# Optimization experiments

Measured on AMD Instinct MI355X. Metric: run time of the kernel, lower is better.

## Reference

```python
import jax, jax.numpy as jnp
import numpy as np

B, T, IN, H = 32, 128, 256, 512      # batch, time, input, hidden
N, R, W = 128, 4, 64                  # mem cells, read heads, cell width
RW = R * W
FOUT = 256
IF = R * W + 3 * W + 5 * R + 3        # DNC interface vector size
EPS = 1e-6


def setup_inputs() -> dict:
    k = jax.random.split(jax.random.key(0), 9)
    g = lambda kk, sh, fan: jax.random.normal(kk, sh, jnp.float32) / np.sqrt(fan).astype(np.float32)
    return {
        "x": jax.random.normal(k[0], (B, T, IN), jnp.float32),
        "W_ih": g(k[1], (4 * H, IN + RW), IN + RW),
        "W_hh": g(k[2], (4 * H, H), H),
        "b_ih": jnp.zeros((4 * H,), jnp.float32),
        "b_hh": jnp.zeros((4 * H,), jnp.float32),
        "W_if": g(k[3], (IF, H), H),
        "b_if": jnp.zeros((IF,), jnp.float32),
        "W_emb": g(k[4], (FOUT, H + RW), H + RW),
        "b_emb": jnp.zeros((FOUT,), jnp.float32),
    }


def _content(keys, strengths, mem):
    # keys (b,k,w), strengths (b,k), mem (b,n,w) -> softmax cosine addressing (b,k,n)
    kn = keys / (jnp.linalg.norm(keys, axis=-1, keepdims=True) + EPS)
    mn = mem / (jnp.linalg.norm(mem, axis=-1, keepdims=True) + EPS)
    sim = jnp.einsum('bkw,bnw->bkn', kn, mn)
    return jax.nn.softmax(sim * strengths[..., None], axis=-1)


def _dnc_forward(x, W_ih, W_hh, b_ih, b_hh, W_if, b_if, W_emb, b_emb):
    b = x.shape[0]
    eye = jnp.eye(N, dtype=x.dtype)

    def step(carry, x_t):
        h, c, mem, link, prec, read_w, write_w, usage, last_read = carry
        # LSTM controller step on [x_t, last_read] (pytorch gate order i,f,g,o)
        inp = jnp.concatenate([x_t, last_read], axis=-1)
        gates = inp @ W_ih.T + h @ W_hh.T + b_ih + b_hh
        i, f, g_, o = jnp.split(gates, 4, axis=-1)
        c = jax.nn.sigmoid(f) * c + jax.nn.sigmoid(i) * jnp.tanh(g_)
        h = jax.nn.sigmoid(o) * jnp.tanh(c)

        # interface vector
        xi = h @ W_if.T + b_if
        off = 0
        read_keys = jnp.tanh(xi[:, :R * W].reshape(b, R, W)); off = R * W
        read_str = jax.nn.softplus(xi[:, off:off + R]); off += R
        write_key = jnp.tanh(xi[:, off:off + W]); off += W
        write_str = jax.nn.softplus(xi[:, off:off + 1]); off += 1
        erase = jax.nn.sigmoid(xi[:, off:off + W]); off += W
        write_vec = jnp.tanh(xi[:, off:off + W]); off += W
        free_g = jax.nn.sigmoid(xi[:, off:off + R]); off += R
        alloc_g = jax.nn.sigmoid(xi[:, off:off + 1]); off += 1
        write_g = jax.nn.sigmoid(xi[:, off:off + 1]); off += 1
        read_modes = jax.nn.softmax(xi[:, off:off + 3 * R].reshape(b, R, 3), axis=-1)

        # usage update + allocation weighting (sort / cumprod / scatter-back)
        psi = jnp.prod(1.0 - free_g[:, :, None] * read_w, axis=1)          # (b,n) retention
        usage = (usage + write_w - usage * write_w) * psi
        order = jnp.argsort(usage, axis=1)                                  # free-list order
        sorted_u = jnp.take_along_axis(usage, order, axis=1)
        cp = jnp.cumprod(jnp.concatenate([jnp.ones((b, 1), usage.dtype), sorted_u[:, :-1]], axis=1), axis=1)
        a_sorted = (1.0 - sorted_u) * cp
        alloc = jnp.zeros_like(usage).at[jnp.arange(b)[:, None], order].set(a_sorted)

        # write weighting + memory update
        cw = _content(write_key[:, None, :], write_str, mem)[:, 0]          # (b,n)
        write_w = write_g * (alloc_g * alloc + (1.0 - alloc_g) * cw)
        mem = mem * (1.0 - write_w[:, :, None] * erase[:, None, :]) + write_w[:, :, None] * write_vec[:, None, :]

        # temporal link matrix + precedence
        link = (1.0 - write_w[:, :, None] - write_w[:, None, :]) * link + write_w[:, :, None] * prec[:, None, :]
        link = link * (1.0 - eye)
        prec = (1.0 - jnp.sum(write_w, axis=1, keepdims=True)) * prec + write_w

        # read weighting: backward / content / forward modes
        fwd = jnp.einsum('bnm,brm->brn', link, read_w)
        bwd = jnp.einsum('bmn,brm->brn', link, read_w)
        cr = _content(read_keys, read_str, mem)
        read_w = read_modes[..., 0:1] * bwd + read_modes[..., 1:2] * cr + read_modes[..., 2:3] * fwd
        read_vecs = jnp.einsum('brn,bnw->brw', read_w, mem)
        last_read = read_vecs.reshape(b, RW)

        out = jnp.concatenate([h, last_read], axis=-1) @ W_emb.T + b_emb
        return (h, c, mem, link, prec, read_w, write_w, usage, last_read), out

    z = jnp.zeros
    carry0 = (z((b, H)), z((b, H)), z((b, N, W)), z((b, N, N)), z((b, N)),
              z((b, R, N)), z((b, N)), z((b, N)), z((b, RW)))
    _, outs = jax.lax.scan(step, carry0, jnp.swapaxes(x, 0, 1))
    return jnp.swapaxes(outs, 0, 1)  # (b, T, FOUT)


def reference(x, W_ih, W_hh, b_ih, b_hh, W_if, b_if, W_emb, b_emb):
    return _dnc_forward(x, W_ih, W_hh, b_ih, b_hh, W_if, b_if, W_emb, b_emb)
```

## Files before the change

kernel.cpp:

```cpp
#include <hip/hip_runtime.h>
#include <math.h>

#define B_    32
#define T_    128
#define IN_   256
#define H_    512
#define N_    128
#define R_    4
#define W_    64
#define RW_   256
#define FOUT_ 256
#define IF_   471
#define XIP   480
#define EPSF  1e-6f
#define KPAD  260
#define NBLK  208

typedef float v4f __attribute__((ext_vector_type(4)));

#define OFF_H0    0
#define OFF_H1    16384
#define OFF_LR    32768
#define OFF_XI    40960
#define OFF_FLAGA (OFF_XI + 32*XIP)
#define OFF_FLAGX (OFF_FLAGA + 144*32)
#define OFF_FLAGC (OFF_FLAGX + 32*32)
#define WS_TOTAL  (OFF_FLAGC + 32*32)

__device__ __forceinline__ float sig_(float x)   { return 1.0f / (1.0f + expf(-x)); }
__device__ __forceinline__ float splus_(float x) { return fmaxf(x, 0.0f) + log1pf(expf(-fabsf(x))); }

__device__ __forceinline__ void cstore(float* p, float v) {
    __hip_atomic_store(p, v, __ATOMIC_RELAXED, __HIP_MEMORY_SCOPE_AGENT);
}
__device__ __forceinline__ unsigned uload(const unsigned* p) {
    return __hip_atomic_load(p, __ATOMIC_RELAXED, __HIP_MEMORY_SCOPE_AGENT);
}
__device__ __forceinline__ void ustore(unsigned* p, unsigned v) {
    __hip_atomic_store(p, v, __ATOMIC_RELAXED, __HIP_MEMORY_SCOPE_AGENT);
}
__device__ __forceinline__ void cload4x4(const float* p0, const float* p1,
                                         const float* p2, const float* p3,
                                         v4f& a, v4f& b, v4f& c, v4f& d) {
    asm volatile(
        "global_load_dwordx4 %0, %4, off sc0 sc1\n\t"
        "global_load_dwordx4 %1, %5, off sc0 sc1\n\t"
        "global_load_dwordx4 %2, %6, off sc0 sc1\n\t"
        "global_load_dwordx4 %3, %7, off sc0 sc1\n\t"
        "s_waitcnt vmcnt(0)"
        : "=&v"(a), "=&v"(b), "=&v"(c), "=&v"(d)
        : "v"(p0), "v"(p1), "v"(p2), "v"(p3)
        : "memory");
}
__device__ __forceinline__ v4f cload4(const float* p) {
    v4f v;
    asm volatile("global_load_dwordx4 %0, %1, off sc0 sc1\n\ts_waitcnt vmcnt(0)"
                 : "=&v"(v) : "v"(p) : "memory");
    return v;
}
__device__ __forceinline__ void cstore4(float* p, v4f v) {
    asm volatile("global_store_dwordx4 %0, %1, off sc0 sc1" :: "v"(p), "v"(v) : "memory");
}

__device__ __forceinline__ unsigned long long shflx64(unsigned long long v, int m) {
    unsigned int lo = (unsigned int)v, hi = (unsigned int)(v >> 32);
    lo = (unsigned int)__shfl_xor((int)lo, m);
    hi = (unsigned int)__shfl_xor((int)hi, m);
    return ((unsigned long long)hi << 32) | lo;
}

__global__ void k_init(float* p, int n) {
    for (int i = blockIdx.x * blockDim.x + threadIdx.x; i < n; i += gridDim.x * blockDim.x)
        p[i] = 0.0f;
}

__device__ __forceinline__ void post_flag(unsigned* slot, unsigned val) {
    asm volatile("s_waitcnt vmcnt(0)" ::: "memory");
    __syncthreads();
    if (threadIdx.x == 0) ustore(slot, val);
}

struct SA {
    float act[32 * KPAD];
    float sg[4][4][32];
    float cc[4][32];
    float hst[4][32];
};
struct SM {
    float link[N_][N_ + 1];
    float mem[N_ * (W_ + 1)];
    float sxi[XIP];
    float rw[R_*N_], fwd[R_*N_], bwd[R_*N_], cr[R_*N_];
    float cw[N_], usage[N_], alloc[N_], wwv[N_], prc[N_], minv[N_];
    float rkeys[R_*W_], wkey[W_], ev[W_], wv[W_];
    float rstr[R_], fg[R_], kinv[R_], m1[R_], modes[R_*3], sc[8];
    unsigned long long key[N_];
};

__device__ __forceinline__ void stage_coh(const float* __restrict__ src, int rowstride,
                                          int colofs, float* lds, int tid) {
    int f0 = 0*256 + tid, f1 = 1*256 + tid, f2 = 2*256 + tid, f3 = 3*256 + tid;
    int f4 = 4*256 + tid, f5 = 5*256 + tid, f6 = 6*256 + tid, f7 = 7*256 + tid;
    const float* p0 = src + (size_t)(f0 >> 6) * rowstride + colofs + ((f0 & 63) << 2);
    const float* p1 = src + (size_t)(f1 >> 6) * rowstride + colofs + ((f1 & 63) << 2);
    const float* p2 = src + (size_t)(f2 >> 6) * rowstride + colofs + ((f2 & 63) << 2);
    const float* p3 = src + (size_t)(f3 >> 6) * rowstride + colofs + ((f3 & 63) << 2);
    const float* p4 = src + (size_t)(f4 >> 6) * rowstride + colofs + ((f4 & 63) << 2);
    const float* p5 = src + (size_t)(f5 >> 6) * rowstride + colofs + ((f5 & 63) << 2);
    const float* p6 = src + (size_t)(f6 >> 6) * rowstride + colofs + ((f6 & 63) << 2);
    const float* p7 = src + (size_t)(f7 >> 6) * rowstride + colofs + ((f7 & 63) << 2);
    v4f r0, r1, r2, r3, r4, r5, r6, r7;
    cload4x4(p0, p1, p2, p3, r0, r1, r2, r3);
    cload4x4(p4, p5, p6, p7, r4, r5, r6, r7);
    *reinterpret_cast<v4f*>(&lds[(f0 >> 6) * KPAD + ((f0 & 63) << 2)]) = r0;
    *reinterpret_cast<v4f*>(&lds[(f1 >> 6) * KPAD + ((f1 & 63) << 2)]) = r1;
    *reinterpret_cast<v4f*>(&lds[(f2 >> 6) * KPAD + ((f2 & 63) << 2)]) = r2;
    *reinterpret_cast<v4f*>(&lds[(f3 >> 6) * KPAD + ((f3 & 63) << 2)]) = r3;
    *reinterpret_cast<v4f*>(&lds[(f4 >> 6) * KPAD + ((f4 & 63) << 2)]) = r4;
    *reinterpret_cast<v4f*>(&lds[(f5 >> 6) * KPAD + ((f5 & 63) << 2)]) = r5;
    *reinterpret_cast<v4f*>(&lds[(f6 >> 6) * KPAD + ((f6 & 63) << 2)]) = r6;
    *reinterpret_cast<v4f*>(&lds[(f7 >> 6) * KPAD + ((f7 & 63) << 2)]) = r7;
}
__device__ __forceinline__ void stage_x(const float* __restrict__ x, int t, float* lds, int tid) {
    #pragma unroll
    for (int i = 0; i < 8; ++i) {
        int f = i * 256 + tid;
        int b = f >> 6, k4 = (f & 63) << 2;
        v4f v = *reinterpret_cast<const v4f*>(x + ((size_t)b * T_ + t) * IN_ + k4);
        *reinterpret_cast<v4f*>(&lds[b * KPAD + k4]) = v;
    }
}

__device__ __forceinline__ void tile_mac4(const float* lds,
        const float* __restrict__ w0p, const float* __restrict__ w1p,
        const float* __restrict__ w2p, const float* __restrict__ w3p,
        int lane, float* v)
{
    v4f w0 = *reinterpret_cast<const v4f*>(w0p + lane * 4);
    v4f w1 = *reinterpret_cast<const v4f*>(w1p + lane * 4);
    v4f w2 = *reinterpret_cast<const v4f*>(w2p + lane * 4);
    v4f w3 = *reinterpret_cast<const v4f*>(w3p + lane * 4);
    #pragma unroll
    for (int b = 0; b < 32; ++b) {
        v4f a = *reinterpret_cast<const v4f*>(lds + b * KPAD + lane * 4);
        v[0*32+b] = fmaf(w0.w, a.w, fmaf(w0.z, a.z, fmaf(w0.y, a.y, fmaf(w0.x, a.x, v[0*32+b]))));
        v[1*32+b] = fmaf(w1.w, a.w, fmaf(w1.z, a.z, fmaf(w1.y, a.y, fmaf(w1.x, a.x, v[1*32+b]))));
        v[2*32+b] = fmaf(w2.w, a.w, fmaf(w2.z, a.z, fmaf(w2.y, a.y, fmaf(w2.x, a.x, v[2*32+b]))));
        v[3*32+b] = fmaf(w3.w, a.w, fmaf(w3.z, a.z, fmaf(w3.y, a.y, fmaf(w3.x, a.x, v[3*32+b]))));
    }
}

__device__ __forceinline__ void fold128(float* v, int lane) {
    #define FOLD_STAGE(D, HALF) { _Pragma("unroll") \
        for (int i = 0; i < HALF; ++i) { \
            float a_ = v[i], c_ = v[i + HALF]; \
            float t_ = (lane & D) ? a_ : c_; \
            t_ = __shfl_xor(t_, D); \
            v[i] = (lane & D) ? (c_ + t_) : (a_ + t_); } }
    FOLD_STAGE(32, 64) FOLD_STAGE(16, 32) FOLD_STAGE(8, 16)
    FOLD_STAGE(4, 8)   FOLD_STAGE(2, 4)   FOLD_STAGE(1, 2)
    #undef FOLD_STAGE
}

__device__ void mem_body(SM& sm, int b, int tid,
        const float* __restrict__ gxi, float* __restrict__ glr)
{
    const int lane = tid & 63, wid = tid >> 6;

    if (tid < 120) {
        v4f v4 = cload4(&gxi[(size_t)b * XIP + tid * 4]);
        *reinterpret_cast<v4f*>(&sm.sxi[tid * 4]) = v4;
    }
    __syncthreads();

    for (int i = tid; i < IF_; i += 256) {
        float vv = sm.sxi[i];
        if      (i < 256) sm.rkeys[i]     = tanhf(vv);
        else if (i < 260) sm.rstr[i-256]  = splus_(vv);
        else if (i < 324) sm.wkey[i-260]  = tanhf(vv);
        else if (i < 325) sm.sc[0]        = splus_(vv);
        else if (i < 389) sm.ev[i-325]    = sig_(vv);
        else if (i < 453) sm.wv[i-389]    = tanhf(vv);
        else if (i < 457) sm.fg[i-453]    = sig_(vv);
        else if (i < 458) sm.sc[1]        = sig_(vv);
        else if (i < 459) sm.sc[2]        = sig_(vv);
        else              sm.modes[i-459] = vv;
    }
    __syncthreads();

    unsigned long long key = ~0ull;
    if (tid < N_) {
        float p = 1.0f;
        #pragma unroll
        for (int r = 0; r < R_; ++r) p *= 1.0f - sm.fg[r] * sm.rw[r*N_ + tid];
        float uo = sm.usage[tid], w0 = sm.wwv[tid];
        float u = (uo + w0 - uo*w0) * p;
        sm.usage[tid] = u;
        unsigned int fb = __float_as_uint(u);
        fb = (fb & 0x80000000u) ? ~fb : (fb | 0x80000000u);
        key = ((unsigned long long)fb << 32) | (unsigned int)tid;
        float s = 0.0f;
        for (int w = 0; w < W_; ++w) { float m = sm.mem[tid*(W_+1)+w]; s += m*m; }
        sm.minv[tid] = 1.0f / (sqrtf(s) + EPSF);
    }
    if (tid >= 128 && tid < 128 + R_) {
        int r = tid - 128;
        float s = 0.0f;
        for (int w = 0; w < W_; ++w) { float kv = sm.rkeys[r*W_+w]; s += kv*kv; }
        sm.kinv[r] = 1.0f / (sqrtf(s) + EPSF);
    }
    if (tid == 132) {
        float s = 0.0f;
        for (int w = 0; w < W_; ++w) s += sm.wkey[w]*sm.wkey[w];
        sm.sc[5] = 1.0f / (sqrtf(s) + EPSF);
    }
    if (tid >= 136 && tid < 136 + R_) {
        int r = tid - 136;
        float m0 = sm.modes[r*3], m1 = sm.modes[r*3+1], m2 = sm.modes[r*3+2];
        float mx = fmaxf(m0, fmaxf(m1, m2));
        float e0 = expf(m0-mx), e1 = expf(m1-mx), e2 = expf(m2-mx);
        float inv = 1.0f / (e0 + e1 + e2);
        sm.modes[r*3] = e0*inv; sm.modes[r*3+1] = e1*inv; sm.modes[r*3+2] = e2*inv;
    }
    __syncthreads();

    if (tid < N_) {
        float d = 0.0f;
        for (int w = 0; w < W_; ++w) d += sm.wkey[w] * sm.mem[tid*(W_+1)+w];
        sm.cw[tid] = d * sm.minv[tid] * sm.sc[5] * sm.sc[0];
    }
    for (int k = 2; k <= N_; k <<= 1) {
        for (int j = k >> 1; j > 0; j >>= 1) {
            unsigned long long pk;
            if (j == 64) {
                if (tid < N_) sm.key[tid] = key;
                __syncthreads();
                pk = (tid < N_) ? sm.key[tid ^ 64] : key;
                __syncthreads();
            } else {
                pk = shflx64(key, j);
            }
            bool lower = (tid & j) == 0;
            bool asc   = (tid & k) == 0;
            if ((key > pk) == (lower == asc)) key = pk;
        }
    }

    float su = 0.0f, ex = 1.0f; int sidx = 0;
    if (tid < N_) {
        sidx = (int)(key & 0xffffffffu);
        su = sm.usage[sidx];
        float p = su;
        #pragma unroll
        for (int off = 1; off < 64; off <<= 1) {
            float pv = __shfl_up(p, off);
            if (lane >= off) p *= pv;
        }
        if (tid == 63) sm.sc[7] = p;
        float e = __shfl_up(p, 1);
        ex = (lane == 0) ? 1.0f : e;
    }
    __syncthreads();
    if (tid < N_) {
        if (tid >= 64) ex *= sm.sc[7];
        sm.alloc[sidx] = (1.0f - su) * ex;
    }
    if (wid == 2) {
        float v0 = sm.cw[lane], v1 = sm.cw[lane+64];
        float m = fmaxf(v0, v1);
        #pragma unroll
        for (int o = 32; o >= 1; o >>= 1) m = fmaxf(m, __shfl_xor(m, o));
        float e0 = expf(v0 - m), e1 = expf(v1 - m);
        float s = e0 + e1;
        #pragma unroll
        for (int o = 32; o >= 1; o >>= 1) s += __shfl_xor(s, o);
        sm.cw[lane] = e0; sm.cw[lane+64] = e1;
        if (lane == 0) sm.sc[4] = 1.0f / s;
    }
    __syncthreads();

    if (tid < N_) {
        float cwn = sm.cw[tid] * sm.sc[4];
        sm.wwv[tid] = sm.sc[2] * (sm.sc[1] * sm.alloc[tid] + (1.0f - sm.sc[1]) * cwn);
    }
    __syncthreads();

    for (int i = tid; i < N_*W_; i += 256) {
        int n = i >> 6, w = i & 63;
        float m = sm.mem[n*(W_+1)+w];
        sm.mem[n*(W_+1)+w] = m * (1.0f - sm.wwv[n]*sm.ev[w]) + sm.wwv[n]*sm.wv[w];
    }
    if (wid == 3) {
        float s = sm.wwv[lane] + sm.wwv[lane+64];
        #pragma unroll
        for (int o = 32; o >= 1; o >>= 1) s += __shfl_xor(s, o);
        if (lane == 0) sm.sc[6] = s;
    }
    __syncthreads();

    for (int i = tid; i < N_*N_; i += 256) {
        int row = i >> 7, col = i & 127;
        float wwr = sm.wwv[row];
        float nv = (1.0f - wwr - sm.wwv[col]) * sm.link[row][col] + wwr * sm.prc[col];
        if (row == col) nv = 0.0f;
        sm.link[row][col] = nv;
    }
    __syncthreads();

    for (int i = tid; i < R_*N_; i += 256) {
        int r = i >> 7, q = i & 127;
        float accf = 0.0f, accb = 0.0f;
        #pragma unroll 4
        for (int m2 = 0; m2 < 128; ++m2) {
            float rv = sm.rw[r*N_ + m2];
            accf = fmaf(sm.link[q][m2], rv, accf);
            accb = fmaf(sm.link[m2][q], rv, accb);
        }
        sm.fwd[i] = accf;
        sm.bwd[i] = accb;
    }
    __syncthreads();

    if (tid < N_) {
        sm.prc[tid] = (1.0f - sm.sc[6]) * sm.prc[tid] + sm.wwv[tid];
        float s = 0.0f;
        for (int w = 0; w < W_; ++w) { float m = sm.mem[tid*(W_+1)+w]; s += m*m; }
        sm.minv[tid] = 1.0f / (sqrtf(s) + EPSF);
    }
    __syncthreads();

    for (int i = tid; i < R_*N_; i += 256) {
        int r = i >> 7, n = i & 127;
        float d = 0.0f;
        for (int w = 0; w < W_; ++w) d += sm.rkeys[r*W_+w] * sm.mem[n*(W_+1)+w];
        sm.cr[i] = d * sm.minv[n] * sm.kinv[r] * sm.rstr[r];
    }
    __syncthreads();

    {
        int r = wid;
        float v0 = sm.cr[r*N_ + lane], v1 = sm.cr[r*N_ + lane + 64];
        float m = fmaxf(v0, v1);
        #pragma unroll
        for (int o = 32; o >= 1; o >>= 1) m = fmaxf(m, __shfl_xor(m, o));
        float e0 = expf(v0 - m), e1 = expf(v1 - m);
        float s = e0 + e1;
        #pragma unroll
        for (int o = 32; o >= 1; o >>= 1) s += __shfl_xor(s, o);
        sm.cr[r*N_ + lane] = e0; sm.cr[r*N_ + lane + 64] = e1;
        if (lane == 0) sm.m1[r] = sm.modes[r*3+1] / s;
    }
    __syncthreads();

    for (int i = tid; i < R_*N_; i += 256) {
        int r = i >> 7;
        sm.rw[i] = sm.modes[r*3] * sm.bwd[i] + sm.m1[r] * sm.cr[i] + sm.modes[r*3+2] * sm.fwd[i];
    }
    __syncthreads();

    for (int i = tid; i < R_*W_; i += 256) {
        int r = i >> 6, w = i & 63;
        float d = 0.0f;
        for (int n = 0; n < N_; ++n) d += sm.rw[r*N_ + n] * sm.mem[n*(W_+1)+w];
        cstore(&glr[(size_t)b * RW_ + i], d);
    }
}

__global__ __launch_bounds__(256, 1) void k_fused(
        const float* __restrict__ x, const float* __restrict__ Wih,
        const float* __restrict__ Whh, const float* __restrict__ bih,
        const float* __restrict__ bhh, const float* __restrict__ Wif,
        const float* __restrict__ bif, const float* __restrict__ Wemb,
        const float* __restrict__ bemb, float* __restrict__ out,
        float* __restrict__ ws)
{
    __shared__ __align__(16) char smem_raw[(sizeof(SM) > sizeof(SA)) ? sizeof(SM) : sizeof(SA)];
    SA& sa = *reinterpret_cast<SA*>(smem_raw);
    SM& sm = *reinterpret_cast<SM*>(smem_raw);

    const int bid = blockIdx.x, tid = threadIdx.x;
    const int lane = tid & 63, wid = tid >> 6;

    float* h0  = ws + OFF_H0;
    float* h1  = ws + OFF_H1;
    float* lr  = ws + OFF_LR;
    float* gxi = ws + OFF_XI;
    unsigned* flagA = (unsigned*)(ws + OFF_FLAGA);
    unsigned* flagX = (unsigned*)(ws + OFF_FLAGX);
    unsigned* flagC = (unsigned*)(ws + OFF_FLAGC);

    if (bid < 128) {
        const int j = bid * 4 + wid;
        if (tid < 128) sa.cc[tid >> 5][tid & 31] = 0.0f;
        float b0 = bih[j]        + bhh[j];
        float b1 = bih[H_ + j]   + bhh[H_ + j];
        float b2 = bih[2*H_ + j] + bhh[2*H_ + j];
        float b3 = bih[3*H_ + j] + bhh[3*H_ + j];
        __syncthreads();

        for (int t = 0; t < T_; ++t) {
            const float* hprev = (t & 1) ? h1 : h0;
            float*       hnew  = (t & 1) ? h0 : h1;
            float v[128];
            #pragma unroll
            for (int i = 0; i < 128; ++i) v[i] = 0.0f;

            stage_x(x, t, sa.act, tid);
            __syncthreads();
            tile_mac4(sa.act, Wih + (size_t)(0*H_+j)*512, Wih + (size_t)(1*H_+j)*512,
                              Wih + (size_t)(2*H_+j)*512, Wih + (size_t)(3*H_+j)*512, lane, v);
            if (tid < 128) { while (uload(&flagA[tid*32]) < (unsigned)t) __builtin_amdgcn_s_sleep(8); }
            __syncthreads();
            stage_coh(hprev, H_, 0, sa.act, tid);
            __syncthreads();
            tile_mac4(sa.act, Whh + (size_t)(0*H_+j)*512, Whh + (size_t)(1*H_+j)*512,
                              Whh + (size_t)(2*H_+j)*512, Whh + (size_t)(3*H_+j)*512, lane, v);
            __syncthreads();
            stage_coh(hprev, H_, 256, sa.act, tid);
            __syncthreads();
            tile_mac4(sa.act, Whh + (size_t)(0*H_+j)*512 + 256, Whh + (size_t)(1*H_+j)*512 + 256,
                              Whh + (size_t)(2*H_+j)*512 + 256, Whh + (size_t)(3*H_+j)*512 + 256, lane, v);
            if (tid < 32) { while (uload(&flagC[tid*32]) < (unsigned)t) __builtin_amdgcn_s_sleep(8); }
            __syncthreads();
            stage_coh(lr, RW_, 0, sa.act, tid);
            __syncthreads();
            tile_mac4(sa.act, Wih + (size_t)(0*H_+j)*512 + 256, Wih + (size_t)(1*H_+j)*512 + 256,
                              Wih + (size_t)(2*H_+j)*512 + 256, Wih + (size_t)(3*H_+j)*512 + 256, lane, v);
            fold128(v, lane);
            int r = (lane >> 4) & 3, bb0 = (lane & 15) * 2;
            sa.sg[wid][r][bb0]     = v[0];
            sa.sg[wid][r][bb0 + 1] = v[1];
            __syncthreads();
            if (lane < 32) {
                int b = lane;
                float ai = sa.sg[wid][0][b] + b0;
                float af = sa.sg[wid][1][b] + b1;
                float ag = sa.sg[wid][2][b] + b2;
                float ao = sa.sg[wid][3][b] + b3;
                float ig = sig_(ai), fg = sig_(af), gg = tanhf(ag), og = sig_(ao);
                float cn = fg * sa.cc[wid][b] + ig * gg;
                sa.cc[wid][b] = cn;
                sa.hst[wid][b] = og * tanhf(cn);
            }
            __syncthreads();
            if (tid < 32) {
                int b = tid;
                v4f hv;
                hv.x = sa.hst[0][b]; hv.y = sa.hst[1][b];
                hv.z = sa.hst[2][b]; hv.w = sa.hst[3][b];
                cstore4(&hnew[(size_t)b * H_ + bid * 4], hv);
            }
            post_flag(&flagA[bid * 32], (unsigned)(t + 1));
        }
    } else if (bid < 144) {
        const int rb = (bid - 128) * 16 + wid * 4;
        const float* w0 = Wemb + (size_t)(rb + 0) * 768;
        const float* w1 = Wemb + (size_t)(rb + 1) * 768;
        const float* w2 = Wemb + (size_t)(rb + 2) * 768;
        const float* w3 = Wemb + (size_t)(rb + 3) * 768;

        for (int t = 0; t < T_; ++t) {
            const float* hprev = (t & 1) ? h1 : h0;
            if (t > 0) {
                float v[128];
                #pragma unroll
                for (int i = 0; i < 128; ++i) v[i] = 0.0f;
                if (tid < 128) { while (uload(&flagA[tid*32]) < (unsigned)t) __builtin_amdgcn_s_sleep(8); }
                __syncthreads();
                stage_coh(hprev, H_, 0, sa.act, tid);
                __syncthreads();
                tile_mac4(sa.act, w0, w1, w2, w3, lane, v);
                __syncthreads();
                stage_coh(hprev, H_, 256, sa.act, tid);
                __syncthreads();
                tile_mac4(sa.act, w0 + 256, w1 + 256, w2 + 256, w3 + 256, lane, v);
                if (tid < 32) { while (uload(&flagC[tid*32]) < (unsigned)t) __builtin_amdgcn_s_sleep(8); }
                __syncthreads();
                stage_coh(lr, RW_, 0, sa.act, tid);
                __syncthreads();
                tile_mac4(sa.act, w0 + 512, w1 + 512, w2 + 512, w3 + 512, lane, v);
                fold128(v, lane);
                int rloc = (lane >> 4) & 3, bb0 = (lane & 15) * 2;
                int row = rb + rloc;
                float bb = bemb[row];
                out[((size_t)bb0       * T_ + (t-1)) * FOUT_ + row] = v[0] + bb;
                out[((size_t)(bb0 + 1) * T_ + (t-1)) * FOUT_ + row] = v[1] + bb;
            }
            post_flag(&flagA[bid * 32], (unsigned)(t + 1));
        }
        {
            if (tid < 32) { while (uload(&flagC[tid*32]) < (unsigned)T_) __builtin_amdgcn_s_sleep(8); }
            __syncthreads();
            float v[128];
            #pragma unroll
            for (int i = 0; i < 128; ++i) v[i] = 0.0f;
            stage_coh(h0, H_, 0, sa.act, tid);
            __syncthreads();
            tile_mac4(sa.act, w0, w1, w2, w3, lane, v);
            __syncthreads();
            stage_coh(h0, H_, 256, sa.act, tid);
            __syncthreads();
            tile_mac4(sa.act, w0 + 256, w1 + 256, w2 + 256, w3 + 256, lane, v);
            __syncthreads();
            stage_coh(lr, RW_, 0, sa.act, tid);
            __syncthreads();
            tile_mac4(sa.act, w0 + 512, w1 + 512, w2 + 512, w3 + 512, lane, v);
            fold128(v, lane);
            int rloc = (lane >> 4) & 3, bb0 = (lane & 15) * 2;
            int row = rb + rloc;
            float bb = bemb[row];
            out[((size_t)bb0       * T_ + (T_-1)) * FOUT_ + row] = v[0] + bb;
            out[((size_t)(bb0 + 1) * T_ + (T_-1)) * FOUT_ + row] = v[1] + bb;
        }
    } else if (bid < 176) {
        const int rb = (bid - 144) * 16 + wid * 4;
        int r0 = min(rb + 0, IF_ - 1), r1 = min(rb + 1, IF_ - 1);
        int r2 = min(rb + 2, IF_ - 1), r3 = min(rb + 3, IF_ - 1);
        const float* w0 = Wif + (size_t)r0 * 512;
        const float* w1 = Wif + (size_t)r1 * 512;
        const float* w2 = Wif + (size_t)r2 * 512;
        const float* w3 = Wif + (size_t)r3 * 512;

        for (int t = 0; t < T_; ++t) {
            float* hnew = (t & 1) ? h0 : h1;
            float v[128];
            #pragma unroll
            for (int i = 0; i < 128; ++i) v[i] = 0.0f;
            if (tid < 128) { while (uload(&flagA[tid*32]) < (unsigned)(t+1)) __builtin_amdgcn_s_sleep(8); }
            __syncthreads();
            stage_coh(hnew, H_, 0, sa.act, tid);
            __syncthreads();
            tile_mac4(sa.act, w0, w1, w2, w3, lane, v);
            __syncthreads();
            stage_coh(hnew, H_, 256, sa.act, tid);
            __syncthreads();
            tile_mac4(sa.act, w0 + 256, w1 + 256, w2 + 256, w3 + 256, lane, v);
            fold128(v, lane);
            int rloc = (lane >> 4) & 3, bb0 = (lane & 15) * 2;
            int row = rb + rloc;
            if (row < IF_) {
                float bb = bif[row];
                cstore(&gxi[(size_t)bb0       * XIP + row], v[0] + bb);
                cstore(&gxi[(size_t)(bb0 + 1) * XIP + row], v[1] + bb);
            }
            post_flag(&flagX[(bid - 144) * 32], (unsigned)(t + 1));
        }
    } else {
        const int b = bid - 176;
        float* z = (float*)&sm;
        for (int i = tid; i < (int)(sizeof(SM)/4); i += 256) z[i] = 0.0f;
        __syncthreads();

        for (int t = 0; t < T_; ++t) {
            unsigned val = (unsigned)(t + 1);
            if (tid < 32) {
                while (uload(&flagX[tid * 32]) < val) __builtin_amdgcn_s_sleep(8);
            } else if (tid >= 64 && tid < 80) {
                while (uload(&flagA[(128 + (tid - 64)) * 32]) < val) __builtin_amdgcn_s_sleep(8);
            }
            __syncthreads();
            mem_body(sm, b, tid, gxi, lr);
            post_flag(&flagC[b * 32], val);
        }
    }
}

extern "C" void kernel_launch(void* const* d_in, const int* in_sizes, int n_in,
                              void* d_out, int out_size, void* d_ws, size_t ws_size,
                              hipStream_t stream)
{
    const float* x    = (const float*)d_in[0];
    const float* Wih  = (const float*)d_in[1];
    const float* Whh  = (const float*)d_in[2];
    const float* bih  = (const float*)d_in[3];
    const float* bhh  = (const float*)d_in[4];
    const float* Wif  = (const float*)d_in[5];
    const float* bif  = (const float*)d_in[6];
    const float* Wemb = (const float*)d_in[7];
    const float* bemb = (const float*)d_in[8];
    float* out = (float*)d_out;
    float* ws  = (float*)d_ws;

    k_init<<<64, 256, 0, stream>>>(ws, WS_TOTAL);

    k_fused<<<dim3(NBLK), dim3(256), 0, stream>>>(x, Wih, Whh, bih, bhh,
                                                  Wif, bif, Wemb, bemb, out, ws);
}
```

Measured before the change: 5.423 ms.

## Double block size to 512 threads and halve persistent block count

```diff
diff --git a/kernel.cpp b/kernel.cpp
--- a/kernel.cpp
+++ b/kernel.cpp
@@ -14,7 +14,12 @@
 #define XIP   480
 #define EPSF  1e-6f
 #define KPAD  260
-#define NBLK  208
+#define NT    512
+#define GB_   64
+#define OB_   8
+#define XB_   15
+#define MB_   32
+#define NBLK  (GB_ + OB_ + XB_ + MB_)
 
 typedef float v4f __attribute__((ext_vector_type(4)));
 
@@ -23,8 +28,8 @@
 #define OFF_LR    32768
 #define OFF_XI    40960
 #define OFF_FLAGA (OFF_XI + 32*XIP)
-#define OFF_FLAGX (OFF_FLAGA + 144*32)
-#define OFF_FLAGC (OFF_FLAGX + 32*32)
+#define OFF_FLAGX (OFF_FLAGA + 72*32)
+#define OFF_FLAGC (OFF_FLAGX + 15*32)
 #define WS_TOTAL  (OFF_FLAGC + 32*32)
 
 __device__ __forceinline__ float sig_(float x)   { return 1.0f / (1.0f + expf(-x)); }
@@ -82,9 +87,9 @@
 
 struct SA {
     float act[32 * KPAD];
-    float sg[4][4][32];
-    float cc[4][32];
-    float hst[4][32];
+    float sg[8][4][32];
+    float cc[8][32];
+    float hst[8][32];
 };
 struct SM {
     float link[N_][N_ + 1];
@@ -99,32 +104,22 @@
 
 __device__ __forceinline__ void stage_coh(const float* __restrict__ src, int rowstride,
                                           int colofs, float* lds, int tid) {
-    int f0 = 0*256 + tid, f1 = 1*256 + tid, f2 = 2*256 + tid, f3 = 3*256 + tid;
-    int f4 = 4*256 + tid, f5 = 5*256 + tid, f6 = 6*256 + tid, f7 = 7*256 + tid;
+    int f0 = 0*NT + tid, f1 = 1*NT + tid, f2 = 2*NT + tid, f3 = 3*NT + tid;
     const float* p0 = src + (size_t)(f0 >> 6) * rowstride + colofs + ((f0 & 63) << 2);
     const float* p1 = src + (size_t)(f1 >> 6) * rowstride + colofs + ((f1 & 63) << 2);
     const float* p2 = src + (size_t)(f2 >> 6) * rowstride + colofs + ((f2 & 63) << 2);
     const float* p3 = src + (size_t)(f3 >> 6) * rowstride + colofs + ((f3 & 63) << 2);
-    const float* p4 = src + (size_t)(f4 >> 6) * rowstride + colofs + ((f4 & 63) << 2);
-    const float* p5 = src + (size_t)(f5 >> 6) * rowstride + colofs + ((f5 & 63) << 2);
-    const float* p6 = src + (size_t)(f6 >> 6) * rowstride + colofs + ((f6 & 63) << 2);
-    const float* p7 = src + (size_t)(f7 >> 6) * rowstride + colofs + ((f7 & 63) << 2);
-    v4f r0, r1, r2, r3, r4, r5, r6, r7;
+    v4f r0, r1, r2, r3;
     cload4x4(p0, p1, p2, p3, r0, r1, r2, r3);
-    cload4x4(p4, p5, p6, p7, r4, r5, r6, r7);
     *reinterpret_cast<v4f*>(&lds[(f0 >> 6) * KPAD + ((f0 & 63) << 2)]) = r0;
     *reinterpret_cast<v4f*>(&lds[(f1 >> 6) * KPAD + ((f1 & 63) << 2)]) = r1;
     *reinterpret_cast<v4f*>(&lds[(f2 >> 6) * KPAD + ((f2 & 63) << 2)]) = r2;
     *reinterpret_cast<v4f*>(&lds[(f3 >> 6) * KPAD + ((f3 & 63) << 2)]) = r3;
-    *reinterpret_cast<v4f*>(&lds[(f4 >> 6) * KPAD + ((f4 & 63) << 2)]) = r4;
-    *reinterpret_cast<v4f*>(&lds[(f5 >> 6) * KPAD + ((f5 & 63) << 2)]) = r5;
-    *reinterpret_cast<v4f*>(&lds[(f6 >> 6) * KPAD + ((f6 & 63) << 2)]) = r6;
-    *reinterpret_cast<v4f*>(&lds[(f7 >> 6) * KPAD + ((f7 & 63) << 2)]) = r7;
 }
 __device__ __forceinline__ void stage_x(const float* __restrict__ x, int t, float* lds, int tid) {
     #pragma unroll
-    for (int i = 0; i < 8; ++i) {
-        int f = i * 256 + tid;
+    for (int i = 0; i < 4; ++i) {
+        int f = i * NT + tid;
         int b = f >> 6, k4 = (f & 63) << 2;
         v4f v = *reinterpret_cast<const v4f*>(x + ((size_t)b * T_ + t) * IN_ + k4);
         *reinterpret_cast<v4f*>(&lds[b * KPAD + k4]) = v;
@@ -173,7 +168,7 @@
     }
     __syncthreads();
 
-    for (int i = tid; i < IF_; i += 256) {
+    for (int i = tid; i < IF_; i += NT) {
         float vv = sm.sxi[i];
         if      (i < 256) sm.rkeys[i]     = tanhf(vv);
         else if (i < 260) sm.rstr[i-256]  = splus_(vv);
@@ -285,7 +280,7 @@
     }
     __syncthreads();
 
-    for (int i = tid; i < N_*W_; i += 256) {
+    for (int i = tid; i < N_*W_; i += NT) {
         int n = i >> 6, w = i & 63;
         float m = sm.mem[n*(W_+1)+w];
         sm.mem[n*(W_+1)+w] = m * (1.0f - sm.wwv[n]*sm.ev[w]) + sm.wwv[n]*sm.wv[w];
@@ -298,7 +293,7 @@
     }
     __syncthreads();
 
-    for (int i = tid; i < N_*N_; i += 256) {
+    for (int i = tid; i < N_*N_; i += NT) {
         int row = i >> 7, col = i & 127;
         float wwr = sm.wwv[row];
         float nv = (1.0f - wwr - sm.wwv[col]) * sm.link[row][col] + wwr * sm.prc[col];
@@ -307,7 +302,7 @@
     }
     __syncthreads();
 
-    for (int i = tid; i < R_*N_; i += 256) {
+    for (int i = tid; i < R_*N_; i += NT) {
         int r = i >> 7, q = i & 127;
         float accf = 0.0f, accb = 0.0f;
         #pragma unroll 4
@@ -329,7 +324,7 @@
     }
     __syncthreads();
 
-    for (int i = tid; i < R_*N_; i += 256) {
+    for (int i = tid; i < R_*N_; i += NT) {
         int r = i >> 7, n = i & 127;
         float d = 0.0f;
         for (int w = 0; w < W_; ++w) d += sm.rkeys[r*W_+w] * sm.mem[n*(W_+1)+w];
@@ -337,7 +332,7 @@
     }
     __syncthreads();
 
-    {
+    if (wid < 4) {
         int r = wid;
         float v0 = sm.cr[r*N_ + lane], v1 = sm.cr[r*N_ + lane + 64];
         float m = fmaxf(v0, v1);
@@ -352,13 +347,13 @@
     }
     __syncthreads();
 
-    for (int i = tid; i < R_*N_; i += 256) {
+    for (int i = tid; i < R_*N_; i += NT) {
         int r = i >> 7;
         sm.rw[i] = sm.modes[r*3] * sm.bwd[i] + sm.m1[r] * sm.cr[i] + sm.modes[r*3+2] * sm.fwd[i];
     }
     __syncthreads();
 
-    for (int i = tid; i < R_*W_; i += 256) {
+    for (int i = tid; i < R_*W_; i += NT) {
         int r = i >> 6, w = i & 63;
         float d = 0.0f;
         for (int n = 0; n < N_; ++n) d += sm.rw[r*N_ + n] * sm.mem[n*(W_+1)+w];
@@ -366,7 +361,7 @@
     }
 }
 
-__global__ __launch_bounds__(256, 1) void k_fused(
+__global__ __launch_bounds__(NT, 1) void k_fused(
         const float* __restrict__ x, const float* __restrict__ Wih,
         const float* __restrict__ Whh, const float* __restrict__ bih,
         const float* __restrict__ bhh, const float* __restrict__ Wif,
@@ -389,9 +384,9 @@
     unsigned* flagX = (unsigned*)(ws + OFF_FLAGX);
     unsigned* flagC = (unsigned*)(ws + OFF_FLAGC);
 
-    if (bid < 128) {
-        const int j = bid * 4 + wid;
-        if (tid < 128) sa.cc[tid >> 5][tid & 31] = 0.0f;
+    if (bid < GB_) {
+        const int j = bid * 8 + wid;
+        if (tid < 256) sa.cc[tid >> 5][tid & 31] = 0.0f;
         float b0 = bih[j]        + bhh[j];
         float b1 = bih[H_ + j]   + bhh[H_ + j];
         float b2 = bih[2*H_ + j] + bhh[2*H_ + j];
@@ -409,7 +404,7 @@
             __syncthreads();
             tile_mac4(sa.act, Wih + (size_t)(0*H_+j)*512, Wih + (size_t)(1*H_+j)*512,
                               Wih + (size_t)(2*H_+j)*512, Wih + (size_t)(3*H_+j)*512, lane, v);
-            if (tid < 128) { while (uload(&flagA[tid*32]) < (unsigned)t) __builtin_amdgcn_s_sleep(8); }
+            if (tid < GB_) { while (uload(&flagA[tid*32]) < (unsigned)t) __builtin_amdgcn_s_sleep(2); }
             __syncthreads();
             stage_coh(hprev, H_, 0, sa.act, tid);
             __syncthreads();
@@ -420,7 +415,7 @@
             __syncthreads();
             tile_mac4(sa.act, Whh + (size_t)(0*H_+j)*512 + 256, Whh + (size_t)(1*H_+j)*512 + 256,
                               Whh + (size_t)(2*H_+j)*512 + 256, Whh + (size_t)(3*H_+j)*512 + 256, lane, v);
-            if (tid < 32) { while (uload(&flagC[tid*32]) < (unsigned)t) __builtin_amdgcn_s_sleep(8); }
+            if (tid < 32) { while (uload(&flagC[tid*32]) < (unsigned)t) __builtin_amdgcn_s_sleep(2); }
             __syncthreads();
             stage_coh(lr, RW_, 0, sa.act, tid);
             __syncthreads();
@@ -431,29 +426,30 @@
             sa.sg[wid][r][bb0]     = v[0];
             sa.sg[wid][r][bb0 + 1] = v[1];
             __syncthreads();
-            if (lane < 32) {
-                int b = lane;
-                float ai = sa.sg[wid][0][b] + b0;
-                float af = sa.sg[wid][1][b] + b1;
-                float ag = sa.sg[wid][2][b] + b2;
-                float ao = sa.sg[wid][3][b] + b3;
+            if (tid < 256) {
+                int jl = tid >> 5, b = tid & 31;
+                int jj = bid * 8 + jl;
+                float ai = sa.sg[jl][0][b] + bih[jj]        + bhh[jj];
+                float af = sa.sg[jl][1][b] + bih[H_ + jj]   + bhh[H_ + jj];
+                float ag = sa.sg[jl][2][b] + bih[2*H_ + jj] + bhh[2*H_ + jj];
+                float ao = sa.sg[jl][3][b] + bih[3*H_ + jj] + bhh[3*H_ + jj];
                 float ig = sig_(ai), fg = sig_(af), gg = tanhf(ag), og = sig_(ao);
-                float cn = fg * sa.cc[wid][b] + ig * gg;
-                sa.cc[wid][b] = cn;
-                sa.hst[wid][b] = og * tanhf(cn);
+                float cn = fg * sa.cc[jl][b] + ig * gg;
+                sa.cc[jl][b] = cn;
+                sa.hst[jl][b] = og * tanhf(cn);
             }
             __syncthreads();
-            if (tid < 32) {
-                int b = tid;
+            if (tid < 64) {
+                int b = tid & 31, half = tid >> 5;
                 v4f hv;
-                hv.x = sa.hst[0][b]; hv.y = sa.hst[1][b];
-                hv.z = sa.hst[2][b]; hv.w = sa.hst[3][b];
-                cstore4(&hnew[(size_t)b * H_ + bid * 4], hv);
+                hv.x = sa.hst[half*4+0][b]; hv.y = sa.hst[half*4+1][b];
+                hv.z = sa.hst[half*4+2][b]; hv.w = sa.hst[half*4+3][b];
+                cstore4(&hnew[(size_t)b * H_ + bid * 8 + half * 4], hv);
             }
             post_flag(&flagA[bid * 32], (unsigned)(t + 1));
         }
-    } else if (bid < 144) {
-        const int rb = (bid - 128) * 16 + wid * 4;
+    } else if (bid < GB_ + OB_) {
+        const int rb = (bid - GB_) * 32 + wid * 4;
         const float* w0 = Wemb + (size_t)(rb + 0) * 768;
         const float* w1 = Wemb + (size_t)(rb + 1) * 768;
         const float* w2 = Wemb + (size_t)(rb + 2) * 768;
@@ -465,7 +461,7 @@
                 float v[128];
                 #pragma unroll
                 for (int i = 0; i < 128; ++i) v[i] = 0.0f;
-                if (tid < 128) { while (uload(&flagA[tid*32]) < (unsigned)t) __builtin_amdgcn_s_sleep(8); }
+                if (tid < GB_) { while (uload(&flagA[tid*32]) < (unsigned)t) __builtin_amdgcn_s_sleep(2); }
                 __syncthreads();
                 stage_coh(hprev, H_, 0, sa.act, tid);
                 __syncthreads();
@@ -474,7 +470,7 @@
                 stage_coh(hprev, H_, 256, sa.act, tid);
                 __syncthreads();
                 tile_mac4(sa.act, w0 + 256, w1 + 256, w2 + 256, w3 + 256, lane, v);
-                if (tid < 32) { while (uload(&flagC[tid*32]) < (unsigned)t) __builtin_amdgcn_s_sleep(8); }
+                if (tid < 32) { while (uload(&flagC[tid*32]) < (unsigned)t) __builtin_amdgcn_s_sleep(2); }
                 __syncthreads();
                 stage_coh(lr, RW_, 0, sa.act, tid);
                 __syncthreads();
@@ -489,7 +485,7 @@
             post_flag(&flagA[bid * 32], (unsigned)(t + 1));
         }
         {
-            if (tid < 32) { while (uload(&flagC[tid*32]) < (unsigned)T_) __builtin_amdgcn_s_sleep(8); }
+            if (tid < 32) { while (uload(&flagC[tid*32]) < (unsigned)T_) __builtin_amdgcn_s_sleep(2); }
             __syncthreads();
             float v[128];
             #pragma unroll
@@ -512,8 +508,8 @@
             out[((size_t)bb0       * T_ + (T_-1)) * FOUT_ + row] = v[0] + bb;
             out[((size_t)(bb0 + 1) * T_ + (T_-1)) * FOUT_ + row] = v[1] + bb;
         }
-    } else if (bid < 176) {
-        const int rb = (bid - 144) * 16 + wid * 4;
+    } else if (bid < GB_ + OB_ + XB_) {
+        const int rb = (bid - GB_ - OB_) * 32 + wid * 4;
         int r0 = min(rb + 0, IF_ - 1), r1 = min(rb + 1, IF_ - 1);
         int r2 = min(rb + 2, IF_ - 1), r3 = min(rb + 3, IF_ - 1);
         const float* w0 = Wif + (size_t)r0 * 512;
@@ -526,7 +522,7 @@
             float v[128];
             #pragma unroll
             for (int i = 0; i < 128; ++i) v[i] = 0.0f;
-            if (tid < 128) { while (uload(&flagA[tid*32]) < (unsigned)(t+1)) __builtin_amdgcn_s_sleep(8); }
+            if (tid < GB_) { while (uload(&flagA[tid*32]) < (unsigned)(t+1)) __builtin_amdgcn_s_sleep(2); }
             __syncthreads();
             stage_coh(hnew, H_, 0, sa.act, tid);
             __syncthreads();
@@ -543,20 +539,20 @@
                 cstore(&gxi[(size_t)bb0       * XIP + row], v[0] + bb);
                 cstore(&gxi[(size_t)(bb0 + 1) * XIP + row], v[1] + bb);
             }
-            post_flag(&flagX[(bid - 144) * 32], (unsigned)(t + 1));
+            post_flag(&flagX[(bid - GB_ - OB_) * 32], (unsigned)(t + 1));
         }
     } else {
-        const int b = bid - 176;
+        const int b = bid - GB_ - OB_ - XB_;
         float* z = (float*)&sm;
-        for (int i = tid; i < (int)(sizeof(SM)/4); i += 256) z[i] = 0.0f;
+        for (int i = tid; i < (int)(sizeof(SM)/4); i += NT) z[i] = 0.0f;
         __syncthreads();
 
         for (int t = 0; t < T_; ++t) {
             unsigned val = (unsigned)(t + 1);
-            if (tid < 32) {
-                while (uload(&flagX[tid * 32]) < val) __builtin_amdgcn_s_sleep(8);
-            } else if (tid >= 64 && tid < 80) {
-                while (uload(&flagA[(128 + (tid - 64)) * 32]) < val) __builtin_amdgcn_s_sleep(8);
+            if (tid < XB_) {
+                while (uload(&flagX[tid * 32]) < val) __builtin_amdgcn_s_sleep(2);
+            } else if (tid >= 32 && tid < 32 + OB_) {
+                while (uload(&flagA[(GB_ + (tid - 32)) * 32]) < val) __builtin_amdgcn_s_sleep(2);
             }
             __syncthreads();
             mem_body(sm, b, tid, gxi, lr);
@@ -583,6 +579,6 @@
 
     k_init<<<64, 256, 0, stream>>>(ws, WS_TOTAL);
 
-    k_fused<<<dim3(NBLK), dim3(256), 0, stream>>>(x, Wih, Whh, bih, bhh,
-                                                  Wif, bif, Wemb, bemb, out, ws);
-}
+    k_fused<<<dim3(NBLK), dim3(NT), 0, stream>>>(x, Wih, Whh, bih, bhh,
+                                                 Wif, bif, Wemb, bemb, out, ws);
+}
```

Result: slower. 7.136 ms (+31.6%).

## Keep weight fragments in registers across timesteps and trim interface blocks

Applied to the files above, without the earlier changes.

```diff
diff --git a/kernel.cpp b/kernel.cpp
--- a/kernel.cpp
+++ b/kernel.cpp
@@ -14,7 +14,12 @@
 #define XIP   480
 #define EPSF  1e-6f
 #define KPAD  260
-#define NBLK  208
+#define NT    256
+#define GB_   128
+#define OB_   16
+#define XB_   30
+#define MB_   32
+#define NBLK  (GB_ + OB_ + XB_ + MB_)
 
 typedef float v4f __attribute__((ext_vector_type(4)));
 
@@ -24,7 +29,7 @@
 #define OFF_XI    40960
 #define OFF_FLAGA (OFF_XI + 32*XIP)
 #define OFF_FLAGX (OFF_FLAGA + 144*32)
-#define OFF_FLAGC (OFF_FLAGX + 32*32)
+#define OFF_FLAGC (OFF_FLAGX + 30*32)
 #define WS_TOTAL  (OFF_FLAGC + 32*32)
 
 __device__ __forceinline__ float sig_(float x)   { return 1.0f / (1.0f + expf(-x)); }
@@ -131,15 +136,9 @@
     }
 }
 
-__device__ __forceinline__ void tile_mac4(const float* lds,
-        const float* __restrict__ w0p, const float* __restrict__ w1p,
-        const float* __restrict__ w2p, const float* __restrict__ w3p,
-        int lane, float* v)
+__device__ __forceinline__ void tile_mac4r(const float* lds,
+        v4f w0, v4f w1, v4f w2, v4f w3, int lane, float* v)
 {
-    v4f w0 = *reinterpret_cast<const v4f*>(w0p + lane * 4);
-    v4f w1 = *reinterpret_cast<const v4f*>(w1p + lane * 4);
-    v4f w2 = *reinterpret_cast<const v4f*>(w2p + lane * 4);
-    v4f w3 = *reinterpret_cast<const v4f*>(w3p + lane * 4);
     #pragma unroll
     for (int b = 0; b < 32; ++b) {
         v4f a = *reinterpret_cast<const v4f*>(lds + b * KPAD + lane * 4);
@@ -148,6 +147,9 @@
         v[2*32+b] = fmaf(w2.w, a.w, fmaf(w2.z, a.z, fmaf(w2.y, a.y, fmaf(w2.x, a.x, v[2*32+b]))));
         v[3*32+b] = fmaf(w3.w, a.w, fmaf(w3.z, a.z, fmaf(w3.y, a.y, fmaf(w3.x, a.x, v[3*32+b]))));
     }
+}
+__device__ __forceinline__ v4f wfrag(const float* p, int lane) {
+    return *reinterpret_cast<const v4f*>(p + lane * 4);
 }
 
 __device__ __forceinline__ void fold128(float* v, int lane) {
@@ -173,7 +175,7 @@
     }
     __syncthreads();
 
-    for (int i = tid; i < IF_; i += 256) {
+    for (int i = tid; i < IF_; i += NT) {
         float vv = sm.sxi[i];
         if      (i < 256) sm.rkeys[i]     = tanhf(vv);
         else if (i < 260) sm.rstr[i-256]  = splus_(vv);
@@ -285,7 +287,7 @@
     }
     __syncthreads();
 
-    for (int i = tid; i < N_*W_; i += 256) {
+    for (int i = tid; i < N_*W_; i += NT) {
         int n = i >> 6, w = i & 63;
         float m = sm.mem[n*(W_+1)+w];
         sm.mem[n*(W_+1)+w] = m * (1.0f - sm.wwv[n]*sm.ev[w]) + sm.wwv[n]*sm.wv[w];
@@ -298,7 +300,7 @@
     }
     __syncthreads();
 
-    for (int i = tid; i < N_*N_; i += 256) {
+    for (int i = tid; i < N_*N_; i += NT) {
         int row = i >> 7, col = i & 127;
         float wwr = sm.wwv[row];
         float nv = (1.0f - wwr - sm.wwv[col]) * sm.link[row][col] + wwr * sm.prc[col];
@@ -307,7 +309,7 @@
     }
     __syncthreads();
 
-    for (int i = tid; i < R_*N_; i += 256) {
+    for (int i = tid; i < R_*N_; i += NT) {
         int r = i >> 7, q = i & 127;
         float accf = 0.0f, accb = 0.0f;
         #pragma unroll 4
@@ -329,7 +331,7 @@
     }
     __syncthreads();
 
-    for (int i = tid; i < R_*N_; i += 256) {
+    for (int i = tid; i < R_*N_; i += NT) {
         int r = i >> 7, n = i & 127;
         float d = 0.0f;
         for (int w = 0; w < W_; ++w) d += sm.rkeys[r*W_+w] * sm.mem[n*(W_+1)+w];
@@ -352,13 +354,13 @@
     }
     __syncthreads();
 
-    for (int i = tid; i < R_*N_; i += 256) {
+    for (int i = tid; i < R_*N_; i += NT) {
         int r = i >> 7;
         sm.rw[i] = sm.modes[r*3] * sm.bwd[i] + sm.m1[r] * sm.cr[i] + sm.modes[r*3+2] * sm.fwd[i];
     }
     __syncthreads();
 
-    for (int i = tid; i < R_*W_; i += 256) {
+    for (int i = tid; i < R_*W_; i += NT) {
         int r = i >> 6, w = i & 63;
         float d = 0.0f;
         for (int n = 0; n < N_; ++n) d += sm.rw[r*N_ + n] * sm.mem[n*(W_+1)+w];
@@ -366,7 +368,7 @@
     }
 }
 
-__global__ __launch_bounds__(256, 1) void k_fused(
+__global__ __launch_bounds__(NT, 1) void k_fused(
         const float* __restrict__ x, const float* __restrict__ Wih,
         const float* __restrict__ Whh, const float* __restrict__ bih,
         const float* __restrict__ bhh, const float* __restrict__ Wif,
@@ -389,13 +391,25 @@
     unsigned* flagX = (unsigned*)(ws + OFF_FLAGX);
     unsigned* flagC = (unsigned*)(ws + OFF_FLAGC);
 
-    if (bid < 128) {
+    if (bid < GB_) {
         const int j = bid * 4 + wid;
+        v4f wA0 = wfrag(Wih + (size_t)(0*H_+j)*512,       lane);
+        v4f wA1 = wfrag(Wih + (size_t)(1*H_+j)*512,       lane);
+        v4f wA2 = wfrag(Wih + (size_t)(2*H_+j)*512,       lane);
+        v4f wA3 = wfrag(Wih + (size_t)(3*H_+j)*512,       lane);
+        v4f wB0 = wfrag(Whh + (size_t)(0*H_+j)*512,       lane);
+        v4f wB1 = wfrag(Whh + (size_t)(1*H_+j)*512,       lane);
+        v4f wB2 = wfrag(Whh + (size_t)(2*H_+j)*512,       lane);
+        v4f wB3 = wfrag(Whh + (size_t)(3*H_+j)*512,       lane);
+        v4f wC0 = wfrag(Whh + (size_t)(0*H_+j)*512 + 256, lane);
+        v4f wC1 = wfrag(Whh + (size_t)(1*H_+j)*512 + 256, lane);
+        v4f wC2 = wfrag(Whh + (size_t)(2*H_+j)*512 + 256, lane);
+        v4f wC3 = wfrag(Whh + (size_t)(3*H_+j)*512 + 256, lane);
+        v4f wD0 = wfrag(Wih + (size_t)(0*H_+j)*512 + 256, lane);
+        v4f wD1 = wfrag(Wih + (size_t)(1*H_+j)*512 + 256, lane);
+        v4f wD2 = wfrag(Wih + (size_t)(2*H_+j)*512 + 256, lane);
+        v4f wD3 = wfrag(Wih + (size_t)(3*H_+j)*512 + 256, lane);
         if (tid < 128) sa.cc[tid >> 5][tid & 31] = 0.0f;
-        float b0 = bih[j]        + bhh[j];
-        float b1 = bih[H_ + j]   + bhh[H_ + j];
-        float b2 = bih[2*H_ + j] + bhh[2*H_ + j];
-        float b3 = bih[3*H_ + j] + bhh[3*H_ + j];
         __syncthreads();
 
         for (int t = 0; t < T_; ++t) {
@@ -407,25 +421,21 @@
 
             stage_x(x, t, sa.act, tid);
             __syncthreads();
-            tile_mac4(sa.act, Wih + (size_t)(0*H_+j)*512, Wih + (size_t)(1*H_+j)*512,
-                              Wih + (size_t)(2*H_+j)*512, Wih + (size_t)(3*H_+j)*512, lane, v);
-            if (tid < 128) { while (uload(&flagA[tid*32]) < (unsigned)t) __builtin_amdgcn_s_sleep(8); }
+            tile_mac4r(sa.act, wA0, wA1, wA2, wA3, lane, v);
+            if (tid < GB_) { while (uload(&flagA[tid*32]) < (unsigned)t) __builtin_amdgcn_s_sleep(1); }
             __syncthreads();
             stage_coh(hprev, H_, 0, sa.act, tid);
             __syncthreads();
-            tile_mac4(sa.act, Whh + (size_t)(0*H_+j)*512, Whh + (size_t)(1*H_+j)*512,
-                              Whh + (size_t)(2*H_+j)*512, Whh + (size_t)(3*H_+j)*512, lane, v);
+            tile_mac4r(sa.act, wB0, wB1, wB2, wB3, lane, v);
             __syncthreads();
             stage_coh(hprev, H_, 256, sa.act, tid);
             __syncthreads();
-            tile_mac4(sa.act, Whh + (size_t)(0*H_+j)*512 + 256, Whh + (size_t)(1*H_+j)*512 + 256,
-                              Whh + (size_t)(2*H_+j)*512 + 256, Whh + (size_t)(3*H_+j)*512 + 256, lane, v);
-            if (tid < 32) { while (uload(&flagC[tid*32]) < (unsigned)t) __builtin_amdgcn_s_sleep(8); }
+            tile_mac4r(sa.act, wC0, wC1, wC2, wC3, lane, v);
+            if (tid < 32) { while (uload(&flagC[tid*32]) < (unsigned)t) __builtin_amdgcn_s_sleep(1); }
             __syncthreads();
             stage_coh(lr, RW_, 0, sa.act, tid);
             __syncthreads();
-            tile_mac4(sa.act, Wih + (size_t)(0*H_+j)*512 + 256, Wih + (size_t)(1*H_+j)*512 + 256,
-                              Wih + (size_t)(2*H_+j)*512 + 256, Wih + (size_t)(3*H_+j)*512 + 256, lane, v);
+            tile_mac4r(sa.act, wD0, wD1, wD2, wD3, lane, v);
             fold128(v, lane);
             int r = (lane >> 4) & 3, bb0 = (lane & 15) * 2;
             sa.sg[wid][r][bb0]     = v[0];
@@ -433,10 +443,11 @@
             __syncthreads();
             if (lane < 32) {
                 int b = lane;
-                float ai = sa.sg[wid][0][b] + b0;
-                float af = sa.sg[wid][1][b] + b1;
-                float ag = sa.sg[wid][2][b] + b2;
-                float ao = sa.sg[wid][3][b] + b3;
+                int jj = j;
+                float ai = sa.sg[wid][0][b] + bih[jj]        + bhh[jj];
+                float af = sa.sg[wid][1][b] + bih[H_ + jj]   + bhh[H_ + jj];
+                float ag = sa.sg[wid][2][b] + bih[2*H_ + jj] + bhh[2*H_ + jj];
+                float ao = sa.sg[wid][3][b] + bih[3*H_ + jj] + bhh[3*H_ + jj];
                 float ig = sig_(ai), fg = sig_(af), gg = tanhf(ag), og = sig_(ao);
                 float cn = fg * sa.cc[wid][b] + ig * gg;
                 sa.cc[wid][b] = cn;
@@ -452,12 +463,20 @@
             }
             post_flag(&flagA[bid * 32], (unsigned)(t + 1));
         }
-    } else if (bid < 144) {
-        const int rb = (bid - 128) * 16 + wid * 4;
-        const float* w0 = Wemb + (size_t)(rb + 0) * 768;
-        const float* w1 = Wemb + (size_t)(rb + 1) * 768;
-        const float* w2 = Wemb + (size_t)(rb + 2) * 768;
-        const float* w3 = Wemb + (size_t)(rb + 3) * 768;
+    } else if (bid < GB_ + OB_) {
+        const int rb = (bid - GB_) * 16 + wid * 4;
+        v4f wA0 = wfrag(Wemb + (size_t)(rb+0)*768,       lane);
+        v4f wA1 = wfrag(Wemb + (size_t)(rb+1)*768,       lane);
+        v4f wA2 = wfrag(Wemb + (size_t)(rb+2)*768,       lane);
+        v4f wA3 = wfrag(Wemb + (size_t)(rb+3)*768,       lane);
+        v4f wB0 = wfrag(Wemb + (size_t)(rb+0)*768 + 256, lane);
+        v4f wB1 = wfrag(Wemb + (size_t)(rb+1)*768 + 256, lane);
+        v4f wB2 = wfrag(Wemb + (size_t)(rb+2)*768 + 256, lane);
+        v4f wB3 = wfrag(Wemb + (size_t)(rb+3)*768 + 256, lane);
+        v4f wC0 = wfrag(Wemb + (size_t)(rb+0)*768 + 512, lane);
+        v4f wC1 = wfrag(Wemb + (size_t)(rb+1)*768 + 512, lane);
+        v4f wC2 = wfrag(Wemb + (size_t)(rb+2)*768 + 512, lane);
+        v4f wC3 = wfrag(Wemb + (size_t)(rb+3)*768 + 512, lane);
 
         for (int t = 0; t < T_; ++t) {
             const float* hprev = (t & 1) ? h1 : h0;
@@ -465,20 +484,20 @@
                 float v[128];
                 #pragma unroll
                 for (int i = 0; i < 128; ++i) v[i] = 0.0f;
-                if (tid < 128) { while (uload(&flagA[tid*32]) < (unsigned)t) __builtin_amdgcn_s_sleep(8); }
+                if (tid < GB_) { while (uload(&flagA[tid*32]) < (unsigned)t) __builtin_amdgcn_s_sleep(1); }
                 __syncthreads();
                 stage_coh(hprev, H_, 0, sa.act, tid);
                 __syncthreads();
-                tile_mac4(sa.act, w0, w1, w2, w3, lane, v);
+                tile_mac4r(sa.act, wA0, wA1, wA2, wA3, lane, v);
                 __syncthreads();
                 stage_coh(hprev, H_, 256, sa.act, tid);
                 __syncthreads();
-                tile_mac4(sa.act, w0 + 256, w1 + 256, w2 + 256, w3 + 256, lane, v);
-                if (tid < 32) { while (uload(&flagC[tid*32]) < (unsigned)t) __builtin_amdgcn_s_sleep(8); }
+                tile_mac4r(sa.act, wB0, wB1, wB2, wB3, lane, v);
+                if (tid < 32) { while (uload(&flagC[tid*32]) < (unsigned)t) __builtin_amdgcn_s_sleep(1); }
                 __syncthreads();
                 stage_coh(lr, RW_, 0, sa.act, tid);
                 __syncthreads();
-                tile_mac4(sa.act, w0 + 512, w1 + 512, w2 + 512, w3 + 512, lane, v);
+                tile_mac4r(sa.act, wC0, wC1, wC2, wC3, lane, v);
                 fold128(v, lane);
                 int rloc = (lane >> 4) & 3, bb0 = (lane & 15) * 2;
                 int row = rb + rloc;
@@ -489,22 +508,22 @@
             post_flag(&flagA[bid * 32], (unsigned)(t + 1));
         }
         {
-            if (tid < 32) { while (uload(&flagC[tid*32]) < (unsigned)T_) __builtin_amdgcn_s_sleep(8); }
+            if (tid < 32) { while (uload(&flagC[tid*32]) < (unsigned)T_) __builtin_amdgcn_s_sleep(1); }
             __syncthreads();
             float v[128];
             #pragma unroll
             for (int i = 0; i < 128; ++i) v[i] = 0.0f;
             stage_coh(h0, H_, 0, sa.act, tid);
             __syncthreads();
-            tile_mac4(sa.act, w0, w1, w2, w3, lane, v);
+            tile_mac4r(sa.act, wA0, wA1, wA2, wA3, lane, v);
             __syncthreads();
             stage_coh(h0, H_, 256, sa.act, tid);
             __syncthreads();
-            tile_mac4(sa.act, w0 + 256, w1 + 256, w2 + 256, w3 + 256, lane, v);
+            tile_mac4r(sa.act, wB0, wB1, wB2, wB3, lane, v);
             __syncthreads();
             stage_coh(lr, RW_, 0, sa.act, tid);
             __syncthreads();
-            tile_mac4(sa.act, w0 + 512, w1 + 512, w2 + 512, w3 + 512, lane, v);
+            tile_mac4r(sa.act, wC0, wC1, wC2, wC3, lane, v);
             fold128(v, lane);
             int rloc = (lane >> 4) & 3, bb0 = (lane & 15) * 2;
             int row = rb + rloc;
@@ -512,29 +531,33 @@
             out[((size_t)bb0       * T_ + (T_-1)) * FOUT_ + row] = v[0] + bb;
             out[((size_t)(bb0 + 1) * T_ + (T_-1)) * FOUT_ + row] = v[1] + bb;
         }
-    } else if (bid < 176) {
-        const int rb = (bid - 144) * 16 + wid * 4;
+    } else if (bid < GB_ + OB_ + XB_) {
+        const int rb = (bid - GB_ - OB_) * 16 + wid * 4;
         int r0 = min(rb + 0, IF_ - 1), r1 = min(rb + 1, IF_ - 1);
         int r2 = min(rb + 2, IF_ - 1), r3 = min(rb + 3, IF_ - 1);
-        const float* w0 = Wif + (size_t)r0 * 512;
-        const float* w1 = Wif + (size_t)r1 * 512;
-        const float* w2 = Wif + (size_t)r2 * 512;
-        const float* w3 = Wif + (size_t)r3 * 512;
+        v4f wA0 = wfrag(Wif + (size_t)r0*512,       lane);
+        v4f wA1 = wfrag(Wif + (size_t)r1*512,       lane);
+        v4f wA2 = wfrag(Wif + (size_t)r2*512,       lane);
+        v4f wA3 = wfrag(Wif + (size_t)r3*512,       lane);
+        v4f wB0 = wfrag(Wif + (size_t)r0*512 + 256, lane);
+        v4f wB1 = wfrag(Wif + (size_t)r1*512 + 256, lane);
+        v4f wB2 = wfrag(Wif + (size_t)r2*512 + 256, lane);
+        v4f wB3 = wfrag(Wif + (size_t)r3*512 + 256, lane);
 
         for (int t = 0; t < T_; ++t) {
             float* hnew = (t & 1) ? h0 : h1;
             float v[128];
             #pragma unroll
             for (int i = 0; i < 128; ++i) v[i] = 0.0f;
-            if (tid < 128) { while (uload(&flagA[tid*32]) < (unsigned)(t+1)) __builtin_amdgcn_s_sleep(8); }
+            if (tid < GB_) { while (uload(&flagA[tid*32]) < (unsigned)(t+1)) __builtin_amdgcn_s_sleep(1); }
             __syncthreads();
             stage_coh(hnew, H_, 0, sa.act, tid);
             __syncthreads();
-            tile_mac4(sa.act, w0, w1, w2, w3, lane, v);
+            tile_mac4r(sa.act, wA0, wA1, wA2, wA3, lane, v);
             __syncthreads();
             stage_coh(hnew, H_, 256, sa.act, tid);
             __syncthreads();
-            tile_mac4(sa.act, w0 + 256, w1 + 256, w2 + 256, w3 + 256, lane, v);
+            tile_mac4r(sa.act, wB0, wB1, wB2, wB3, lane, v);
             fold128(v, lane);
             int rloc = (lane >> 4) & 3, bb0 = (lane & 15) * 2;
             int row = rb + rloc;
@@ -543,20 +566,20 @@
                 cstore(&gxi[(size_t)bb0       * XIP + row], v[0] + bb);
                 cstore(&gxi[(size_t)(bb0 + 1) * XIP + row], v[1] + bb);
             }
-            post_flag(&flagX[(bid - 144) * 32], (unsigned)(t + 1));
+            post_flag(&flagX[(bid - GB_ - OB_) * 32], (unsigned)(t + 1));
         }
     } else {
-        const int b = bid - 176;
+        const int b = bid - GB_ - OB_ - XB_;
         float* z = (float*)&sm;
-        for (int i = tid; i < (int)(sizeof(SM)/4); i += 256) z[i] = 0.0f;
+        for (int i = tid; i < (int)(sizeof(SM)/4); i += NT) z[i] = 0.0f;
         __syncthreads();
 
         for (int t = 0; t < T_; ++t) {
             unsigned val = (unsigned)(t + 1);
-            if (tid < 32) {
-                while (uload(&flagX[tid * 32]) < val) __builtin_amdgcn_s_sleep(8);
-            } else if (tid >= 64 && tid < 80) {
-                while (uload(&flagA[(128 + (tid - 64)) * 32]) < val) __builtin_amdgcn_s_sleep(8);
+            if (tid < XB_) {
+                while (uload(&flagX[tid * 32]) < val) __builtin_amdgcn_s_sleep(1);
+            } else if (tid >= 32 && tid < 32 + OB_) {
+                while (uload(&flagA[(GB_ + (tid - 32)) * 32]) < val) __builtin_amdgcn_s_sleep(1);
             }
             __syncthreads();
             mem_body(sm, b, tid, gxi, lr);
@@ -583,6 +606,6 @@
 
     k_init<<<64, 256, 0, stream>>>(ws, WS_TOTAL);
 
-    k_fused<<<dim3(NBLK), dim3(256), 0, stream>>>(x, Wih, Whh, bih, bhh,
-                                                  Wif, bif, Wemb, bemb, out, ws);
-}
+    k_fused<<<dim3(NBLK), dim3(NT), 0, stream>>>(x, Wih, Whh, bih, bhh,
+                                                 Wif, bif, Wemb, bemb, out, ws);
+}
```

Result: no change. 5.526 ms (+1.9%).
